# Performance work log

Hardware: AMD Instinct MI355X
Metric: run time of the kernel (lower is better)

## Reference

```python
import jax, jax.numpy as jnp
import numpy as np

EPS = 1e-5

def _ln(x, g, b):
    m = jnp.mean(x, axis=-1, keepdims=True)
    v = jnp.mean((x - m) ** 2, axis=-1, keepdims=True)
    return (x - m) / jnp.sqrt(v + EPS) * g + b

B, SX, SY = 2, 2048, 2048
XD, YD, P, H, MULT = 1024, 1024, 64, 16, 4

def setup_inputs() -> dict:
    key = jax.random.key(0)
    ks = jax.random.split(key, 20)
    s = lambda fan: 1.0 / np.sqrt(fan)
    return {
        "x": jax.random.normal(ks[0], (B, SX, XD), jnp.float32),
        "y": jax.random.normal(ks[1], (B, SY, YD), jnp.float32),
        "gx_gamma": jnp.ones((XD,), jnp.float32),
        "gx_beta": jnp.zeros((XD,), jnp.float32),
        "gy_gamma": jnp.ones((YD,), jnp.float32),
        "gy_beta": jnp.zeros((YD,), jnp.float32),
        "Wq": jax.random.uniform(ks[2], (H, XD, P), jnp.float32, -s(XD), s(XD)),
        "bq": jax.random.uniform(ks[3], (H, P), jnp.float32, -s(XD), s(XD)),
        "Wk": jax.random.uniform(ks[4], (H, YD, P), jnp.float32, -s(YD), s(YD)),
        "bk": jax.random.uniform(ks[5], (H, P), jnp.float32, -s(YD), s(YD)),
        "Wv": jax.random.uniform(ks[6], (H, YD, P), jnp.float32, -s(YD), s(YD)),
        "bv": jax.random.uniform(ks[7], (H, P), jnp.float32, -s(YD), s(YD)),
        "Wo": jax.random.uniform(ks[8], (H * P, XD), jnp.float32, -s(H * P), s(H * P)),
        "bo": jax.random.uniform(ks[9], (XD,), jnp.float32, -s(H * P), s(H * P)),
        "gd_gamma": jnp.ones((XD,), jnp.float32),
        "gd_beta": jnp.zeros((XD,), jnp.float32),
        "W1": jax.random.uniform(ks[10], (XD, MULT * XD), jnp.float32, -s(XD), s(XD)),
        "b1": jax.random.uniform(ks[11], (MULT * XD,), jnp.float32, -s(XD), s(XD)),
        "W2": jax.random.uniform(ks[12], (MULT * XD, XD), jnp.float32, -s(MULT * XD), s(MULT * XD)),
        "b2": jax.random.uniform(ks[13], (XD,), jnp.float32, -s(MULT * XD), s(MULT * XD)),
        "mask": 1,
    }

def reference(x, y, gx_gamma, gx_beta, gy_gamma, gy_beta, Wq, bq, Wk, bk, Wv, bv,
              Wo, bo, gd_gamma, gd_beta, W1, b1, W2, b2, mask):
    xn = _ln(x, gx_gamma, gx_beta)
    yn = _ln(y, gy_gamma, gy_beta)
    # batched per-head projections: [B,S,D] x [H,D,P] -> [B,H,S,P]
    q = jnp.einsum('bsd,hdp->bhsp', xn, Wq) + bq[None, :, None, :]
    k = jnp.einsum('btd,hdp->bhtp', yn, Wk) + bk[None, :, None, :]
    v = jnp.einsum('btd,hdp->bhtp', yn, Wv) + bv[None, :, None, :]
    scores = jnp.einsum('bhsp,bhtp->bhst', q, k) * (1.0 / jnp.sqrt(jnp.float32(P)))
    attn = jax.nn.softmax(scores, axis=-1)
    if mask:
        # post-softmax strictly-upper-triangular mask (torch.triu diagonal=1)
        tri = jnp.triu(jnp.ones((SX, SY), attn.dtype), k=1)
        attn = attn * tri
    o = jnp.einsum('bhst,bhtp->bhsp', attn, v)          # [B,H,S,P]
    o = o.transpose(0, 2, 1, 3).reshape(B, SX, H * P)    # concat heads
    x2 = x + o @ Wo + bo
    h = jax.nn.gelu(_ln(x2, gd_gamma, gd_beta) @ W1 + b1, approximate=False)
    return x2 + h @ W2 + b2
```

## Files before the change

### kernel.cpp

```cpp
#include <hip/hip_runtime.h>
#include <hip/hip_bf16.h>
#include <math.h>

typedef __bf16 bf16_t;
typedef __bf16 bf16x8 __attribute__((ext_vector_type(8)));
typedef __bf16 bf16x4 __attribute__((ext_vector_type(4)));
typedef float f32x4 __attribute__((ext_vector_type(4)));

#define QSCALE 0.18033688011112042f

static __device__ __forceinline__ f32x4 mfma16(bf16x8 a, bf16x8 b, f32x4 c) {
  return __builtin_amdgcn_mfma_f32_16x16x32_bf16(a, b, c, 0, 0, 0);
}

static __device__ __forceinline__ float gelu_f(float x) {
  return 0.5f * x * (1.0f + erff(x * 0.70710678118654752440f));
}

static __device__ __forceinline__ float exp2_fast(float x) {
  float r;
  asm("v_exp_f32 %0, %1" : "=v"(r) : "v"(x));
  return r;
}

typedef __attribute__((address_space(1))) const void as1_void;
typedef __attribute__((address_space(3))) void as3_void;
static __device__ __forceinline__ void gload16(const void* g, void* s) {
  __builtin_amdgcn_global_load_lds((as1_void*)g, (as3_void*)s, 16, 0, 0);
}

static __device__ __forceinline__ long hmi(int row, int col) {
  return ((((long)(row >> 11) * 16 + (col >> 6)) * 2048) + (row & 2047)) * 64 + (col & 63);
}

__global__ __launch_bounds__(256) void prep_all(
    const float* __restrict__ Wq, const float* __restrict__ Wk, const float* __restrict__ Wv,
    const float* __restrict__ Wo, const float* __restrict__ W1, const float* __restrict__ W2,
    bf16_t* __restrict__ WqkvT, bf16_t* __restrict__ WoT, bf16_t* __restrict__ W1T,
    bf16_t* __restrict__ W2T, const float* __restrict__ x, const float* __restrict__ y,
    const float* __restrict__ gx, const float* __restrict__ bex, const float* __restrict__ gy,
    const float* __restrict__ bey, bf16_t* __restrict__ xn, bf16_t* __restrict__ yn) {
  const int bid = blockIdx.x;
  if (bid >= 3072) {
    const int lrow = bid - 3072;
    const float* in = lrow < 4096 ? x : y;
    const float* g = lrow < 4096 ? gx : gy;
    const float* be = lrow < 4096 ? bex : bey;
    bf16_t* out = lrow < 4096 ? xn : yn;
    const int row = lrow & 4095;
    const int t = threadIdx.x;
    const float4 xv = ((const float4*)(in + (long)row * 1024))[t];
    float s1 = xv.x + xv.y + xv.z + xv.w;
    float s2 = xv.x * xv.x + xv.y * xv.y + xv.z * xv.z + xv.w * xv.w;
#pragma unroll
    for (int m = 1; m < 64; m <<= 1) {
      s1 += __shfl_xor(s1, m);
      s2 += __shfl_xor(s2, m);
    }
    __shared__ float r1[4], r2[4];
    if ((t & 63) == 0) { r1[t >> 6] = s1; r2[t >> 6] = s2; }
    __syncthreads();
    s1 = r1[0] + r1[1] + r1[2] + r1[3];
    s2 = r2[0] + r2[1] + r2[2] + r2[3];
    const float mean = s1 * (1.0f / 1024.0f);
    float var = s2 * (1.0f / 1024.0f) - mean * mean;
    const float rstd = rsqrtf(fmaxf(var, 0.0f) + 1e-5f);
    const float4 gv = ((const float4*)g)[t];
    const float4 bv = ((const float4*)be)[t];
    bf16x4 o;
    o[0] = (bf16_t)((xv.x - mean) * rstd * gv.x + bv.x);
    o[1] = (bf16_t)((xv.y - mean) * rstd * gv.y + bv.y);
    o[2] = (bf16_t)((xv.z - mean) * rstd * gv.z + bv.z);
    o[3] = (bf16_t)((xv.w - mean) * rstd * gv.w + bv.w);
    *(bf16x4*)(out + (long)row * 1024 + t * 4) = o;
    return;
  }
  const float* inp;
  bf16_t* outp;
  int istride, ostride, i0, j0;
  if (bid < 768) {
    const int wsel = bid >> 8, rem = bid & 255;
    const int h = rem >> 4, xt = rem & 15;
    const float* W = wsel == 0 ? Wq : (wsel == 1 ? Wk : Wv);
    inp = W + h * 65536;
    outp = WqkvT + (long)wsel * 1048576 + h * 65536;
    istride = 64; ostride = 1024; i0 = xt * 64; j0 = 0;
  } else if (bid < 1024) {
    const int rem = bid - 768;
    inp = Wo; outp = WoT; istride = 1024; ostride = 1024;
    i0 = (rem & 15) * 64; j0 = (rem >> 4) * 64;
  } else if (bid < 2048) {
    const int rem = bid - 1024;
    inp = W1; outp = W1T; istride = 4096; ostride = 1024;
    i0 = (rem & 15) * 64; j0 = (rem >> 4) * 64;
  } else {
    const int rem = bid - 2048;
    inp = W2; outp = W2T; istride = 1024; ostride = 4096;
    i0 = (rem >> 4) * 64; j0 = (rem & 15) * 64;
  }
  __shared__ bf16_t tile[64][65];
  const int r = threadIdx.x >> 2, cs = (threadIdx.x & 3) * 16;
#pragma unroll
  for (int jj = 0; jj < 16; jj++)
    tile[cs + jj][r] = (bf16_t)inp[(long)(i0 + r) * istride + j0 + cs + jj];
  __syncthreads();
#pragma unroll
  for (int jj = 0; jj < 16; jj++)
    outp[(long)(j0 + r) * ostride + i0 + cs + jj] = tile[r][cs + jj];
}

__global__ __launch_bounds__(256) void ln_kernel(const float* __restrict__ in,
                                                 const float* __restrict__ g,
                                                 const float* __restrict__ be,
                                                 bf16_t* __restrict__ out) {
  const int row = blockIdx.x, t = threadIdx.x;
  const float4 xv = ((const float4*)(in + (long)row * 1024))[t];
  float s1 = xv.x + xv.y + xv.z + xv.w;
  float s2 = xv.x * xv.x + xv.y * xv.y + xv.z * xv.z + xv.w * xv.w;
#pragma unroll
  for (int m = 1; m < 64; m <<= 1) {
    s1 += __shfl_xor(s1, m);
    s2 += __shfl_xor(s2, m);
  }
  __shared__ float r1[4], r2[4];
  if ((t & 63) == 0) { r1[t >> 6] = s1; r2[t >> 6] = s2; }
  __syncthreads();
  s1 = r1[0] + r1[1] + r1[2] + r1[3];
  s2 = r2[0] + r2[1] + r2[2] + r2[3];
  const float mean = s1 * (1.0f / 1024.0f);
  float var = s2 * (1.0f / 1024.0f) - mean * mean;
  const float rstd = rsqrtf(fmaxf(var, 0.0f) + 1e-5f);
  const float4 gv = ((const float4*)g)[t];
  const float4 bv = ((const float4*)be)[t];
  bf16x4 o;
  o[0] = (bf16_t)((xv.x - mean) * rstd * gv.x + bv.x);
  o[1] = (bf16_t)((xv.y - mean) * rstd * gv.y + bv.y);
  o[2] = (bf16_t)((xv.z - mean) * rstd * gv.z + bv.z);
  o[3] = (bf16_t)((xv.w - mean) * rstd * gv.w + bv.w);
  *(bf16x4*)(out + (long)row * 1024 + t * 4) = o;
}

template <int EPI, int BN>
__global__ __launch_bounds__(256) void gemm32(const bf16_t* __restrict__ A,
                                              const bf16_t* __restrict__ A2,
                                              const bf16_t* __restrict__ Bt,
                                              const float* __restrict__ bias,
                                              const float* __restrict__ biasB,
                                              const float* __restrict__ biasC,
                                              bf16_t* __restrict__ aux,
                                              void* __restrict__ Cout,
                                              int M, int N, int K) {
  constexpr int NF = BN / 32;
  constexpr int NBI = BN / 64;
  __shared__ bf16_t a_lds[2][128 * 32];
  __shared__ bf16_t b_lds[2][BN * 32];
  const int tid = threadIdx.x, l = tid & 63, w = tid >> 6;
  const int wr = w >> 1, wc = w & 1;
  const int nwg = gridDim.x * gridDim.y;
  const int orig = blockIdx.y * gridDim.x + blockIdx.x;
  const int lid = (orig & 7) * (nwg >> 3) + (orig >> 3);
  const int bx = lid % gridDim.x, by = lid / gridDim.x;
  const int m0 = by * 128, n0 = bx * BN;
  const bf16_t* Ause = (EPI == 5 && n0 >= 1024) ? A2 : A;
  const int lr = l & 15, lg = l >> 4;
  long a_src[2];
  int a_dst[2];
#pragma unroll
  for (int i = 0; i < 2; i++) {
    const int row = i * 64 + (tid >> 2);
    const int sc = ((tid & 3) ^ ((row >> 1) & 3)) * 8;
    a_src[i] = (long)(m0 + row) * K + sc;
    a_dst[i] = (i * 64 + w * 16) * 32;
  }
  long b_src[NBI];
#pragma unroll
  for (int i = 0; i < NBI; i++) {
    const int row = i * 64 + (tid >> 2);
    const int sc = ((tid & 3) ^ ((row >> 1) & 3)) * 8;
    b_src[i] = (long)(n0 + row) * K + sc;
  }
  const int nk = K >> 5;
  f32x4 acc[4][NF] = {};
#pragma unroll
  for (int i = 0; i < 2; i++) gload16(Ause + a_src[i], &a_lds[0][a_dst[i]]);
#pragma unroll
  for (int i = 0; i < NBI; i++) gload16(Bt + b_src[i], &b_lds[0][a_dst[i]]);
  __syncthreads();
  int cur = 0;
  for (int t = 0; t < nk; t++) {
    if (t + 1 < nk) {
      const long k0 = (long)(t + 1) * 32;
#pragma unroll
      for (int i = 0; i < 2; i++) gload16(Ause + a_src[i] + k0, &a_lds[cur ^ 1][a_dst[i]]);
#pragma unroll
      for (int i = 0; i < NBI; i++) gload16(Bt + b_src[i] + k0, &b_lds[cur ^ 1][a_dst[i]]);
    }
    const char* ab = (const char*)&a_lds[cur][0];
    const char* bb = (const char*)&b_lds[cur][0];
    bf16x8 af[4], bfr[NF];
#pragma unroll
    for (int m = 0; m < 4; m++) {
      const int row = wr * 64 + m * 16 + lr;
      af[m] = *(const bf16x8*)(ab + row * 64 + 16 * (lg ^ ((row >> 1) & 3)));
    }
#pragma unroll
    for (int n = 0; n < NF; n++) {
      const int row = wc * (BN / 2) + n * 16 + lr;
      bfr[n] = *(const bf16x8*)(bb + row * 64 + 16 * (lg ^ ((row >> 1) & 3)));
    }
    __builtin_amdgcn_s_setprio(1);
#pragma unroll
    for (int m = 0; m < 4; m++)
#pragma unroll
      for (int n = 0; n < NF; n++) acc[m][n] = mfma16(af[m], bfr[n], acc[m][n]);
    __builtin_amdgcn_s_setprio(0);
    __syncthreads();
    cur ^= 1;
  }
#pragma unroll
  for (int m = 0; m < 4; m++)
#pragma unroll
    for (int n = 0; n < NF; n++) {
      const int row_b = m0 + wr * 64 + m * 16 + (l >> 4) * 4;
      const int col = n0 + wc * (BN / 2) + n * 16 + lr;
      if (EPI == 2) {
        const float bia = bias[col];
#pragma unroll
        for (int r = 0; r < 4; r++) {
          const long idx = (long)(row_b + r) * N + col;
          ((bf16_t*)Cout)[idx] = (bf16_t)gelu_f(acc[m][n][r] + bia);
        }
      } else if (EPI == 5) {
        if (col < 1024) {
          const float bia = bias[col];
#pragma unroll
          for (int r = 0; r < 4; r++)
            ((bf16_t*)Cout)[hmi(row_b + r, col)] = (bf16_t)((acc[m][n][r] + bia) * QSCALE);
        } else if (col < 2048) {
          const float bia = biasB[col - 1024];
#pragma unroll
          for (int r = 0; r < 4; r++)
            ((bf16_t*)Cout + 4194304)[hmi(row_b + r, col - 1024)] =
                (bf16_t)(acc[m][n][r] + bia);
        } else {
          const int vcol = col - 2048;
          const float bia = biasC[vcol];
          bf16x4 vv;
#pragma unroll
          for (int r = 0; r < 4; r++) vv[r] = (bf16_t)(acc[m][n][r] + bia);
          const int bb2 = row_b >> 11, tt = row_b & 2047;
          *(bf16x4*)&aux[(((long)(bb2 << 4) + (vcol >> 6)) * 64 + (vcol & 63)) * 2048 + tt] = vv;
        }
      }
    }
}

template <int EPI, int BN>
__global__ __launch_bounds__(256) void gemm64(const bf16_t* __restrict__ A,
                                              const bf16_t* __restrict__ Bt,
                                              const float* __restrict__ bias,
                                              const float* __restrict__ res,
                                              void* __restrict__ Cout,
                                              int M, int N, int K) {
  constexpr int NF = BN / 32;
  constexpr int NBI = BN / 32;
  __shared__ bf16_t a_lds[2][128 * 64];
  __shared__ bf16_t b_lds[2][BN * 64];
  const int tid = threadIdx.x, l = tid & 63, w = tid >> 6;
  const int wr = w >> 1, wc = w & 1;
  const int nwg = gridDim.x * gridDim.y;
  const int orig = blockIdx.y * gridDim.x + blockIdx.x;
  const int lid = (orig & 7) * (nwg >> 3) + (orig >> 3);
  const int bx = lid % gridDim.x, by = lid / gridDim.x;
  const int m0 = by * 128, n0 = bx * BN;
  const int lr = l & 15, lg = l >> 4;
  long a_src[4];
  int ldst[4];
#pragma unroll
  for (int i = 0; i < 4; i++) {
    const int row = i * 32 + w * 8 + (l >> 3);
    const int sc = ((l & 7) ^ (row & 7)) * 8;
    a_src[i] = (long)(m0 + row) * K + sc;
    ldst[i] = (i * 32 + w * 8) * 64;
  }
  long b_src[NBI];
#pragma unroll
  for (int i = 0; i < NBI; i++) {
    const int row = i * 32 + w * 8 + (l >> 3);
    const int sc = ((l & 7) ^ (row & 7)) * 8;
    b_src[i] = (long)(n0 + row) * K + sc;
  }
  const int nk = K >> 6;
  f32x4 acc[4][NF] = {};
#pragma unroll
  for (int i = 0; i < 4; i++) gload16(A + a_src[i], &a_lds[0][ldst[i]]);
#pragma unroll
  for (int i = 0; i < NBI; i++) gload16(Bt + b_src[i], &b_lds[0][ldst[i]]);
  __syncthreads();
  const int sw = (lr & 7) << 4;
  int cur = 0;
  for (int t = 0; t < nk; t++) {
    if (t + 1 < nk) {
      const long k0 = (long)(t + 1) * 64;
#pragma unroll
      for (int i = 0; i < 4; i++) gload16(A + a_src[i] + k0, &a_lds[cur ^ 1][ldst[i]]);
#pragma unroll
      for (int i = 0; i < NBI; i++) gload16(Bt + b_src[i] + k0, &b_lds[cur ^ 1][ldst[i]]);
    }
    const char* ab = (const char*)&a_lds[cur][0];
    const char* bb = (const char*)&b_lds[cur][0];
    bf16x8 af[4][2], bfr[NF][2];
#pragma unroll
    for (int m = 0; m < 4; m++) {
      const int rb = (wr * 64 + m * 16 + lr) * 128;
      af[m][0] = *(const bf16x8*)(ab + rb + ((16 * lg) ^ sw));
      af[m][1] = *(const bf16x8*)(ab + rb + ((16 * lg + 64) ^ sw));
    }
#pragma unroll
    for (int n = 0; n < NF; n++) {
      const int rb = (wc * (BN / 2) + n * 16 + lr) * 128;
      bfr[n][0] = *(const bf16x8*)(bb + rb + ((16 * lg) ^ sw));
      bfr[n][1] = *(const bf16x8*)(bb + rb + ((16 * lg + 64) ^ sw));
    }
    __builtin_amdgcn_s_setprio(1);
#pragma unroll
    for (int kk = 0; kk < 2; kk++)
#pragma unroll
      for (int m = 0; m < 4; m++)
#pragma unroll
        for (int n = 0; n < NF; n++)
          acc[m][n] = mfma16(af[m][kk], bfr[n][kk], acc[m][n]);
    __builtin_amdgcn_s_setprio(0);
    __syncthreads();
    cur ^= 1;
  }
#pragma unroll
  for (int m = 0; m < 4; m++)
#pragma unroll
    for (int n = 0; n < NF; n++) {
      const int row_b = m0 + wr * 64 + m * 16 + (l >> 4) * 4;
      const int col = n0 + wc * (BN / 2) + n * 16 + lr;
      const float bia = bias[col];
#pragma unroll
      for (int r = 0; r < 4; r++) {
        const long idx = (long)(row_b + r) * N + col;
        ((float*)Cout)[idx] = acc[m][n][r] + bia + res[idx];
      }
    }
}

__global__ __launch_bounds__(256) void attn_kernel(const bf16_t* __restrict__ qhm,
                                                   const bf16_t* __restrict__ khm,
                                                   const bf16_t* __restrict__ vtg,
                                                   bf16_t* __restrict__ og,
                                                   const int* __restrict__ maskp) {
  const int T = 2048, HP = 1024;
  __shared__ bf16_t k_lds[2][64 * 64];
  __shared__ bf16_t vt_lds[2][64 * 64];
  __shared__ bf16_t p_lds[4 * 32 * 72];
  const int bh = blockIdx.x, b = bh >> 4, h = bh & 15;
  const int q0 = blockIdx.y * 128;
  const int tid = threadIdx.x, l = tid & 63, w = tid >> 6;
  const int lr = l & 15, lg = l >> 4, lg4 = lg * 4;
  const int srow0 = q0 + w * 32 + lr;
  const bf16_t* kbase = khm + (long)bh * T * 64;
  const bf16_t* vbase = vtg + (long)bh * 64 * T;
  bf16x8 qf[2][2];
#pragma unroll
  for (int g = 0; g < 2; g++) {
    const bf16_t* qr = qhm + ((long)bh * 2048 + srow0 + g * 16) * 64 + lg * 8;
    qf[g][0] = *(const bf16x8*)qr;
    qf[g][1] = *(const bf16x8*)(qr + 32);
  }
  bf16_t* pl = &p_lds[w * 32 * 72];
  float lpart[2] = {0.0f, 0.0f};
  f32x4 oat[4][2] = {};

  const int swz = (lr & 7) << 4;
  const int fo0 = lr * 128 + ((16 * lg) ^ swz);
  const int fo1 = lr * 128 + ((64 + 16 * lg) ^ swz);

  const bool do_mask = (maskp[0] != 0);
  const int nM = do_mask ? (q0 >> 6) : 0;
  const int nt = T >> 6;

  const int sch = l & 7, srow8 = l >> 3;
  int cur = 0;
  {
    const bool needV = (nM == 0);
#pragma unroll
    for (int i = 0; i < 2; i++) {
      const int row = (i * 4 + w) * 8 + srow8;
      const int sc = (sch ^ (row & 7)) * 8;
      gload16(kbase + (long)row * 64 + sc, &k_lds[0][(i * 4 + w) * 512]);
      if (needV) gload16(vbase + (long)row * 2048 + 0 + sc, &vt_lds[0][(i * 4 + w) * 512]);
    }
  }
  __syncthreads();

  for (int t = 0; t < nt; t++) {
    const int t0 = t << 6;
    const int mode = (t < nM) ? 0 : ((do_mask && t < nM + 2) ? 1 : 2);
    if (t + 1 < nt) {
      const int t1 = (t + 1) << 6;
      const bool needV = (t + 1) >= nM;
#pragma unroll
      for (int i = 0; i < 2; i++) {
        const int row = (i * 4 + w) * 8 + srow8;
        const int sc = (sch ^ (row & 7)) * 8;
        gload16(kbase + (long)(t1 + row) * 64 + sc, &k_lds[cur ^ 1][(i * 4 + w) * 512]);
        if (needV)
          gload16(vbase + (long)row * 2048 + t1 + sc, &vt_lds[cur ^ 1][(i * 4 + w) * 512]);
      }
    }
    const char* kb = (const char*)&k_lds[cur][0];
    f32x4 sacc[4][2];
    __builtin_amdgcn_s_setprio(1);
#pragma unroll
    for (int n = 0; n < 4; n++) {
      bf16x8 kf0 = *(const bf16x8*)(kb + n * 2048 + fo0);
      bf16x8 kf1 = *(const bf16x8*)(kb + n * 2048 + fo1);
#pragma unroll
      for (int g = 0; g < 2; g++) {
        f32x4 z = {0.0f, 0.0f, 0.0f, 0.0f};
        z = mfma16(kf0, qf[g][0], z);
        sacc[n][g] = mfma16(kf1, qf[g][1], z);
      }
    }
    __builtin_amdgcn_s_setprio(0);
    float pv[2][4][4];
#pragma unroll
    for (int g = 0; g < 2; g++) {
      float psn[4];
#pragma unroll
      for (int n = 0; n < 4; n++) {
        pv[g][n][0] = exp2_fast(sacc[n][g][0]);
        pv[g][n][1] = exp2_fast(sacc[n][g][1]);
        pv[g][n][2] = exp2_fast(sacc[n][g][2]);
        pv[g][n][3] = exp2_fast(sacc[n][g][3]);
        psn[n] = (pv[g][n][0] + pv[g][n][1]) + (pv[g][n][2] + pv[g][n][3]);
      }
      lpart[g] += (psn[0] + psn[1]) + (psn[2] + psn[3]);
    }
    if (mode > 0) {
#pragma unroll
      for (int g = 0; g < 2; g++)
#pragma unroll
        for (int n = 0; n < 4; n++) {
          bf16x4 pk;
#pragma unroll
          for (int r = 0; r < 4; r++) {
            float v = pv[g][n][r];
            if (mode == 1 && (t0 + n * 16 + lg4 + r) <= srow0 + g * 16) v = 0.0f;
            pk[r] = (bf16_t)v;
          }
          *(bf16x4*)&pl[(g * 16 + lr) * 72 + n * 16 + lg4] = pk;
        }
      const char* vtb = (const char*)&vt_lds[cur][0];
      __builtin_amdgcn_s_setprio(1);
#pragma unroll
      for (int kk = 0; kk < 2; kk++) {
        bf16x8 pb0 = *(bf16x8*)&pl[lr * 72 + kk * 32 + lg * 8];
        bf16x8 pb1 = *(bf16x8*)&pl[(16 + lr) * 72 + kk * 32 + lg * 8];
        const int fkk = lr * 128 + ((kk * 64 + 16 * lg) ^ swz);
#pragma unroll
        for (int np = 0; np < 4; np++) {
          bf16x8 vtf = *(const bf16x8*)(vtb + np * 2048 + fkk);
          oat[np][0] = mfma16(vtf, pb0, oat[np][0]);
          oat[np][1] = mfma16(vtf, pb1, oat[np][1]);
        }
      }
      __builtin_amdgcn_s_setprio(0);
    }
    __syncthreads();
    cur ^= 1;
  }
  float inv[2];
#pragma unroll
  for (int g = 0; g < 2; g++) {
    float lsum = lpart[g];
    lsum += __shfl_xor(lsum, 16);
    lsum += __shfl_xor(lsum, 32);
    inv[g] = 1.0f / lsum;
  }
#pragma unroll
  for (int g = 0; g < 2; g++)
#pragma unroll
    for (int np = 0; np < 4; np++) {
      bf16x4 o4;
#pragma unroll
      for (int r = 0; r < 4; r++) o4[r] = (bf16_t)(oat[np][g][r] * inv[g]);
      *(bf16x4*)&pl[(g * 16 + lr) * 72 + np * 16 + lg4] = o4;
    }
  const int es = l >> 2, ec = (l & 3) * 16;
#pragma unroll
  for (int g = 0; g < 2; g++) {
    bf16x8 o0 = *(bf16x8*)&pl[(g * 16 + es) * 72 + ec];
    bf16x8 o1 = *(bf16x8*)&pl[(g * 16 + es) * 72 + ec + 8];
    bf16_t* orow = og + (long)(b * 2048 + q0 + w * 32 + g * 16 + es) * HP + h * 64 + ec;
    *(bf16x8*)&orow[0] = o0;
    *(bf16x8*)&orow[8] = o1;
  }
}

extern "C" void kernel_launch(void* const* d_in, const int* in_sizes, int n_in,
                              void* d_out, int out_size, void* d_ws, size_t ws_size,
                              hipStream_t stream) {
  const float* x = (const float*)d_in[0];
  const float* y = (const float*)d_in[1];
  const float* gxg = (const float*)d_in[2];
  const float* gxb = (const float*)d_in[3];
  const float* gyg = (const float*)d_in[4];
  const float* gyb = (const float*)d_in[5];
  const float* Wq = (const float*)d_in[6];
  const float* bq = (const float*)d_in[7];
  const float* Wk = (const float*)d_in[8];
  const float* bk = (const float*)d_in[9];
  const float* Wv = (const float*)d_in[10];
  const float* bv = (const float*)d_in[11];
  const float* Wo = (const float*)d_in[12];
  const float* bo = (const float*)d_in[13];
  const float* gdg = (const float*)d_in[14];
  const float* gdb = (const float*)d_in[15];
  const float* W1 = (const float*)d_in[16];
  const float* b1 = (const float*)d_in[17];
  const float* W2 = (const float*)d_in[18];
  const float* b2 = (const float*)d_in[19];
  const int* maskp = (const int*)d_in[20];
  float* out = (float*)d_out;

  char* ws = (char*)d_ws;
  const long MB = 1024 * 1024;
  bf16_t* xn = (bf16_t*)(ws + 0);
  bf16_t* yn = (bf16_t*)(ws + 8 * MB);
  bf16_t* WqkvT = (bf16_t*)(ws + 16 * MB);
  bf16_t* WoT = (bf16_t*)(ws + 22 * MB);
  bf16_t* W1T = (bf16_t*)(ws + 24 * MB);
  bf16_t* W2T = (bf16_t*)(ws + 32 * MB);
  bf16_t* qhm = (bf16_t*)(ws + 40 * MB);
  bf16_t* vTb = (bf16_t*)(ws + 64 * MB);
  bf16_t* ob = (bf16_t*)(ws + 0);
  bf16_t* xd = (bf16_t*)(ws + 8 * MB);
  bf16_t* hb = (bf16_t*)(ws + 40 * MB);
  bf16_t* khm = qhm + 4194304;

  prep_all<<<11264, 256, 0, stream>>>(Wq, Wk, Wv, Wo, W1, W2, WqkvT, WoT, W1T, W2T, x, y, gxg,
                                      gxb, gyg, gyb, xn, yn);
  gemm32<5, 128><<<dim3(24, 32), 256, 0, stream>>>(xn, yn, WqkvT, bq, bk, bv, vTb, qhm, 4096,
                                                   3072, 1024);
  attn_kernel<<<dim3(32, 16), 256, 0, stream>>>(qhm, khm, vTb, ob, maskp);
  gemm64<1, 64><<<dim3(16, 32), 256, 0, stream>>>(ob, WoT, bo, x, out, 4096, 1024, 1024);
  ln_kernel<<<4096, 256, 0, stream>>>(out, gdg, gdb, xd);
  gemm32<2, 128><<<dim3(32, 32), 256, 0, stream>>>(xd, nullptr, W1T, b1, nullptr, nullptr,
                                                   nullptr, hb, 4096, 4096, 1024);
  gemm64<1, 64><<<dim3(16, 32), 256, 0, stream>>>(hb, W2T, b2, out, out, 4096, 1024, 4096);
}
```

Baseline: 251.0 us.

## Triple-buffer gemm32 LDS pipeline and remap tiles per XCD for L2 locality

The gemm32 kernel moves from double to triple LDS buffering. Loads are issued two k-steps ahead, and completion is tracked with explicit vmcnt waits plus a single barrier per iteration, replacing the trailing __syncthreads. Tile-to-XCD assignment is also changed so each XCD handles a contiguous rectangular block of tiles (RW columns wide), with the aim of better L2 reuse. The cost is more LDS per block, which may lower occupancy, and the hand-coded vmcnt count depends on exactly 4 loads per stage.

```diff
diff --git a/kernel.cpp b/kernel.cpp
--- a/kernel.cpp
+++ b/kernel.cpp
@@ -140,7 +140,7 @@
   *(bf16x4*)(out + (long)row * 1024 + t * 4) = o;
 }
 
-template <int EPI, int BN>
+template <int EPI, int BN, int RW>
 __global__ __launch_bounds__(256) void gemm32(const bf16_t* __restrict__ A,
                                               const bf16_t* __restrict__ A2,
                                               const bf16_t* __restrict__ Bt,
@@ -152,14 +152,17 @@
                                               int M, int N, int K) {
   constexpr int NF = BN / 32;
   constexpr int NBI = BN / 64;
-  __shared__ bf16_t a_lds[2][128 * 32];
-  __shared__ bf16_t b_lds[2][BN * 32];
+  __shared__ bf16_t a_lds[3][128 * 32];
+  __shared__ bf16_t b_lds[3][BN * 32];
   const int tid = threadIdx.x, l = tid & 63, w = tid >> 6;
   const int wr = w >> 1, wc = w & 1;
   const int nwg = gridDim.x * gridDim.y;
   const int orig = blockIdx.y * gridDim.x + blockIdx.x;
-  const int lid = (orig & 7) * (nwg >> 3) + (orig >> 3);
-  const int bx = lid % gridDim.x, by = lid / gridDim.x;
+  const int cpx = nwg >> 3;
+  const int xcd = orig & 7, ii = orig >> 3;
+  const int rpr = gridDim.x / RW;
+  const int bx = (xcd % rpr) * RW + (ii % RW);
+  const int by = (xcd / rpr) * (cpx / RW) + (ii / RW);
   const int m0 = by * 128, n0 = bx * BN;
   const bf16_t* Ause = (EPI == 5 && n0 >= 1024) ? A2 : A;
   const int lr = l & 15, lg = l >> 4;
@@ -182,21 +185,28 @@
   const int nk = K >> 5;
   f32x4 acc[4][NF] = {};
 #pragma unroll
-  for (int i = 0; i < 2; i++) gload16(Ause + a_src[i], &a_lds[0][a_dst[i]]);
-#pragma unroll
-  for (int i = 0; i < NBI; i++) gload16(Bt + b_src[i], &b_lds[0][a_dst[i]]);
-  __syncthreads();
-  int cur = 0;
+  for (int tt = 0; tt < 2; tt++) {
+#pragma unroll
+    for (int i = 0; i < 2; i++) gload16(Ause + a_src[i] + tt * 32, &a_lds[tt][a_dst[i]]);
+#pragma unroll
+    for (int i = 0; i < NBI; i++) gload16(Bt + b_src[i] + tt * 32, &b_lds[tt][a_dst[i]]);
+  }
+  int cu = 0;
   for (int t = 0; t < nk; t++) {
-    if (t + 1 < nk) {
-      const long k0 = (long)(t + 1) * 32;
-#pragma unroll
-      for (int i = 0; i < 2; i++) gload16(Ause + a_src[i] + k0, &a_lds[cur ^ 1][a_dst[i]]);
-#pragma unroll
-      for (int i = 0; i < NBI; i++) gload16(Bt + b_src[i] + k0, &b_lds[cur ^ 1][a_dst[i]]);
-    }
-    const char* ab = (const char*)&a_lds[cur][0];
-    const char* bb = (const char*)&b_lds[cur][0];
+    if (t + 1 < nk) asm volatile("s_waitcnt vmcnt(4)" ::: "memory");
+    else            asm volatile("s_waitcnt vmcnt(0)" ::: "memory");
+    __builtin_amdgcn_s_barrier();
+    __builtin_amdgcn_sched_barrier(0);
+    if (t + 2 < nk) {
+      const long k0 = (long)(t + 2) * 32;
+      const int nb = cu >= 1 ? cu - 1 : 2;
+#pragma unroll
+      for (int i = 0; i < 2; i++) gload16(Ause + a_src[i] + k0, &a_lds[nb][a_dst[i]]);
+#pragma unroll
+      for (int i = 0; i < NBI; i++) gload16(Bt + b_src[i] + k0, &b_lds[nb][a_dst[i]]);
+    }
+    const char* ab = (const char*)&a_lds[cu][0];
+    const char* bb = (const char*)&b_lds[cu][0];
     bf16x8 af[4], bfr[NF];
 #pragma unroll
     for (int m = 0; m < 4; m++) {
@@ -214,8 +224,7 @@
 #pragma unroll
       for (int n = 0; n < NF; n++) acc[m][n] = mfma16(af[m], bfr[n], acc[m][n]);
     __builtin_amdgcn_s_setprio(0);
-    __syncthreads();
-    cur ^= 1;
+    cu = cu < 2 ? cu + 1 : 0;
   }
 #pragma unroll
   for (int m = 0; m < 4; m++)
@@ -546,12 +555,12 @@
 
   prep_all<<<11264, 256, 0, stream>>>(Wq, Wk, Wv, Wo, W1, W2, WqkvT, WoT, W1T, W2T, x, y, gxg,
                                       gxb, gyg, gyb, xn, yn);
-  gemm32<5, 128><<<dim3(24, 32), 256, 0, stream>>>(xn, yn, WqkvT, bq, bk, bv, vTb, qhm, 4096,
-                                                   3072, 1024);
+  gemm32<5, 128, 12><<<dim3(24, 32), 256, 0, stream>>>(xn, yn, WqkvT, bq, bk, bv, vTb, qhm,
+                                                       4096, 3072, 1024);
   attn_kernel<<<dim3(32, 16), 256, 0, stream>>>(qhm, khm, vTb, ob, maskp);
   gemm64<1, 64><<<dim3(16, 32), 256, 0, stream>>>(ob, WoT, bo, x, out, 4096, 1024, 1024);
   ln_kernel<<<4096, 256, 0, stream>>>(out, gdg, gdb, xd);
-  gemm32<2, 128><<<dim3(32, 32), 256, 0, stream>>>(xd, nullptr, W1T, b1, nullptr, nullptr,
-                                                   nullptr, hb, 4096, 4096, 1024);
+  gemm32<2, 128, 16><<<dim3(32, 32), 256, 0, stream>>>(xd, nullptr, W1T, b1, nullptr, nullptr,
+                                                       nullptr, hb, 4096, 4096, 1024);
   gemm64<1, 64><<<dim3(16, 32), 256, 0, stream>>>(hb, W2T, b2, out, out, 4096, 1024, 4096);
 }
```

Result: no change. 249.5 us (-0.6%).
